# Performance work log

Hardware: AMD Instinct MI355X
Metric: run time of the kernel (lower is better)

## Reference

```python
import jax, jax.numpy as jnp
import numpy as np

# dims: batch, q-heads, kv-heads, seq, head_dim, block size, window (kv blocks per q block)
B, H, KVH, S, D = 2, 16, 4, 4096, 64
BLK, W = 64, 8
G = H // KVH          # heads per group = 4
NQ = S // BLK         # 64 query blocks
L = W * BLK           # flattened kv window per q block = 512


def setup_inputs() -> dict:
    key = jax.random.key(0)
    k0, k1, k2, k3 = jax.random.split(key, 4)
    q = jax.random.normal(k0, (B, H, S, D), jnp.float32)
    k = jax.random.normal(k1, (B, KVH, S, D), jnp.float32)
    v = jax.random.normal(k2, (B, KVH, S, D), jnp.float32)
    # standard alibi slopes 2^(-8i/H)
    alibi_slopes = jnp.asarray(2.0 ** (-8.0 * np.arange(1, H + 1) / H), jnp.float32)
    # contiguous segments via sorted random ids
    segment_ids = jnp.sort(jax.random.randint(k3, (B, S), 0, 8, jnp.int32), axis=-1)
    # causal sliding window: q block qb attends to kv blocks [qb-W+1, qb]; -1 = invalid
    qb = np.arange(NQ)[:, None]
    bi = qb - (W - 1) + np.arange(W)[None, :]
    block_indices = jnp.asarray(np.where(bi < 0, -1, bi), jnp.int32)  # [NQ, W]
    return {"q": q, "k": k, "v": v, "alibi_slopes": alibi_slopes,
            "segment_ids": segment_ids, "block_indices": block_indices}


def reference(q, k, v, alibi_slopes, segment_ids, block_indices):
    scale = jnp.float32(1.0 / np.sqrt(D))
    NEG = jnp.float32(-1e30)

    qg = q.reshape(B, KVH, G, NQ, BLK, D)          # GQA grouping
    kb = k.reshape(B, KVH, NQ, BLK, D)
    vb = v.reshape(B, KVH, NQ, BLK, D)

    safe = jnp.clip(block_indices, 0)               # [NQ, W]
    kg = kb[:, :, safe]                             # [B,KVH,NQ,W,BLK,D] gathered kv blocks
    vg = vb[:, :, safe]

    pos_m = (jnp.arange(NQ) * BLK)[:, None] + jnp.arange(BLK)             # [NQ,BM]
    pos_n = safe[:, :, None] * BLK + jnp.arange(BLK)[None, None, :]       # [NQ,W,BN]

    valid = (block_indices >= 0)[:, None, :, None]                        # [NQ,1,W,1]
    causal = pos_m[:, :, None, None] >= pos_n[:, None, :, :]              # [NQ,BM,W,BN]
    seg_q = segment_ids.reshape(B, NQ, BLK)
    seg_k = jnp.take(segment_ids, pos_n.reshape(-1), axis=1).reshape(B, NQ, W, BLK)
    same_seg = (seg_q[:, :, :, None, None] == seg_k[:, :, None, :, :]) & (seg_q[:, :, :, None, None] >= 0)
    mask = ((valid & causal)[None] & same_seg)                            # [B,NQ,BM,W,BN]
    maskb = mask.reshape(B, 1, 1, NQ, BLK, L)                             # broadcast over KVH,G

    scores = jnp.einsum('bkgqmd,bkqwnd->bkgqmwn', qg, kg) * scale         # [B,KVH,G,NQ,BM,W,BN]
    pos_diff = jnp.abs(pos_m[:, :, None, None] - pos_n[:, None, :, :]).astype(jnp.float32)
    scores = scores - alibi_slopes.reshape(KVH, G)[None, :, :, None, None, None, None] * pos_diff
    scores = scores.reshape(B, KVH, G, NQ, BLK, L)
    scores = jnp.where(maskb, scores, NEG)

    row_max = jnp.max(scores, axis=-1, keepdims=True)
    p = jnp.where(maskb, jnp.exp(scores - row_max), 0.0)
    l = jnp.sum(p, axis=-1, keepdims=True)                                # [B,KVH,G,NQ,BM,1]
    vf = vg.reshape(B, KVH, NQ, L, D)
    acc = jnp.einsum('bkgqml,bkqld->bkgqmd', p, vf)
    out = jnp.where(l > 0, acc / jnp.where(l > 0, l, 1.0), 0.0)           # zero rows with no valid kv
    return out.reshape(B, H, S, D)
```

## Files before the change

kernel.cpp:

```cpp
#include <hip/hip_runtime.h>
#include <hip/hip_bf16.h>

#define NKVH 4
#define SEQ 4096
#define BLK 64
#define NW 8
#define NQB 64

typedef __attribute__((ext_vector_type(8))) short bf16x8;
typedef __attribute__((ext_vector_type(4))) float f32x4;

__device__ __forceinline__ unsigned pkbf(unsigned lo, unsigned hi) {
  return __builtin_amdgcn_perm(hi + 0x8000u, lo + 0x8000u, 0x07060302u);
}

__device__ __forceinline__ void gload16(const void* g, void* l) {
  __builtin_amdgcn_global_load_lds(
      (const __attribute__((address_space(1))) void*)g,
      (__attribute__((address_space(3))) void*)l, 16, 0, 0);
}

__global__ __launch_bounds__(256, 2)
void prep_kernel(const float* __restrict__ kp, const float* __restrict__ vp,
                 short* __restrict__ kw, short* __restrict__ vt)
{
  const int ki = blockIdx.x, kvh = blockIdx.y, b = blockIdx.z;
  const size_t base = (((size_t)(b*NKVH + kvh)*SEQ) + (size_t)ki*BLK)*64;
  __shared__ float sk[64][72];
  __shared__ float sv[64][72];
  const int t = threadIdx.x;
  #pragma unroll
  for (int it = 0; it < 4; ++it) {
    const int i = t + it*256;
    const int row = i >> 4, c4 = i & 15;
    float4 a = *(const float4*)(kp + base + row*64 + c4*4);
    *(float4*)&sk[row][c4*4] = a;
    float4 v = *(const float4*)(vp + base + row*64 + c4*4);
    *(float4*)&sv[row][c4*4] = v;
  }
  __syncthreads();
  #pragma unroll
  for (int it = 0; it < 2; ++it) {
    const int o = t + it*256;
    const int s = o >> 8, fd = (o >> 6) & 3, lg = (o >> 4) & 3, lr = o & 15;
    const int krow = 8*(lr >> 2) + (lr & 3) + 4*(fd & 1) + 32*(fd >> 1);
    const float* src = &sk[krow][s*32 + lg*8];
    uint4 w;
    w.x = pkbf(__float_as_uint(src[0]), __float_as_uint(src[1]));
    w.y = pkbf(__float_as_uint(src[2]), __float_as_uint(src[3]));
    w.z = pkbf(__float_as_uint(src[4]), __float_as_uint(src[5]));
    w.w = pkbf(__float_as_uint(src[6]), __float_as_uint(src[7]));
    *(uint4*)(kw + base + (size_t)o*8) = w;
    const int d = fd*16 + lr;
    const int n0 = s*32 + lg*8;
    uint4 u;
    u.x = pkbf(__float_as_uint(sv[n0+0][d]), __float_as_uint(sv[n0+1][d]));
    u.y = pkbf(__float_as_uint(sv[n0+2][d]), __float_as_uint(sv[n0+3][d]));
    u.z = pkbf(__float_as_uint(sv[n0+4][d]), __float_as_uint(sv[n0+5][d]));
    u.w = pkbf(__float_as_uint(sv[n0+6][d]), __float_as_uint(sv[n0+7][d]));
    *(uint4*)(vt + base + (size_t)o*8) = u;
  }
}

__global__ __launch_bounds__(256, 2)
void sattn_kernel(const float* __restrict__ qp, const short* __restrict__ kw,
                  const short* __restrict__ vt, const float* __restrict__ alibi,
                  const int* __restrict__ seg, const int* __restrict__ bidx,
                  float* __restrict__ outp)
{
  const int raw = blockIdx.x;
  const int xcd = raw & 7, li = raw >> 3;
  const int b = xcd >> 2, kvh = xcd & 3;
  const int qb = li & 63, hp = li >> 6;

  const int tid = threadIdx.x;
  const int wave = tid >> 6, lane = tid & 63;
  const int lr = lane & 15, lg = lane >> 4;
  const int wh = wave & 1, wq = wave >> 1;
  const int head = kvh*4 + hp*2 + wh;

  __shared__ short klds[2][4096];
  __shared__ short vlds[2][4096];

  int kis[NW];
  #pragma unroll
  for (int i = 0; i < NW; ++i) kis[i] = bidx[qb*NW + i];

  int m_glob[2], mloc[2], sq[2];
  #pragma unroll
  for (int g = 0; g < 2; ++g) {
    mloc[g] = (wq*2 + g)*16 + lr;
    m_glob[g] = qb*BLK + mloc[g];
    sq[g] = seg[b*SEQ + m_glob[g]];
  }
  const float LOG2E = 1.4426950408889634f;
  const float nslope = -alibi[head] * LOG2E;

  const short* kbase = kw + ((size_t)(b*NKVH + kvh)*SEQ)*64;
  const short* vbase = vt + ((size_t)(b*NKVH + kvh)*SEQ)*64;

  auto STAGE = [&](int buf, int wi) {
    const int ki = kis[wi] < 0 ? 0 : kis[wi];
    const char* ksrc = (const char*)(kbase + (size_t)ki*4096);
    const char* vsrc = (const char*)(vbase + (size_t)ki*4096);
    gload16(ksrc + tid*16,        (char*)&klds[buf][0] + wave*1024);
    gload16(ksrc + 4096 + tid*16, (char*)&klds[buf][0] + 4096 + wave*1024);
    gload16(vsrc + tid*16,        (char*)&vlds[buf][0] + wave*1024);
    gload16(vsrc + 4096 + tid*16, (char*)&vlds[buf][0] + 4096 + wave*1024);
  };

  STAGE(0, 0);

  bf16x8 qf[2][2];
  {
    const float qs = 0.125f * LOG2E;
    #pragma unroll
    for (int g = 0; g < 2; ++g) {
      const float* qrow = qp + (((size_t)b*16 + head)*SEQ + m_glob[g])*64;
      #pragma unroll
      for (int s = 0; s < 2; ++s) {
        float4 a = *(const float4*)(qrow + s*32 + lg*8);
        float4 c = *(const float4*)(qrow + s*32 + lg*8 + 4);
        union { unsigned u[4]; bf16x8 v; } cv;
        cv.u[0] = pkbf(__float_as_uint(a.x*qs), __float_as_uint(a.y*qs));
        cv.u[1] = pkbf(__float_as_uint(a.z*qs), __float_as_uint(a.w*qs));
        cv.u[2] = pkbf(__float_as_uint(c.x*qs), __float_as_uint(c.y*qs));
        cv.u[3] = pkbf(__float_as_uint(c.z*qs), __float_as_uint(c.w*qs));
        qf[g][s] = cv.v;
      }
    }
  }

  union { unsigned short us[8]; bf16x8 v; } one_u;
  #pragma unroll
  for (int i = 0; i < 8; ++i) one_u.us[i] = 0x3F80;
  const bf16x8 onesf = one_u.v;

  f32x4 oacc[2][4], osum[2];
  #pragma unroll
  for (int g = 0; g < 2; ++g) {
    f32x4 z = {0.f,0.f,0.f,0.f};
    osum[g] = z;
    #pragma unroll
    for (int dt = 0; dt < 4; ++dt) oacc[g][dt] = z;
  }

  __syncthreads();

  int cur = 0;
  #pragma unroll
  for (int wi = 0; wi < NW; ++wi) {
    if (wi + 1 < NW) STAGE(cur ^ 1, wi + 1);
    const int ki = kis[wi];
    if (ki >= 0) {
      int skr[4][4];
      #pragma unroll
      for (int f = 0; f < 4; ++f) {
        const int nb = lg*8 + 4*(f & 1) + 32*(f >> 1);
        const int4 s4 = *(const int4*)(seg + b*SEQ + ki*BLK + nb);
        skr[f][0] = s4.x; skr[f][1] = s4.y; skr[f][2] = s4.z; skr[f][3] = s4.w;
      }

      f32x4 sacc[2][4];
      #pragma unroll
      for (int g = 0; g < 2; ++g)
        #pragma unroll
        for (int f = 0; f < 4; ++f) { f32x4 z = {0.f,0.f,0.f,0.f}; sacc[g][f] = z; }
      #pragma unroll
      for (int s = 0; s < 2; ++s) {
        bf16x8 kf[4];
        #pragma unroll
        for (int f = 0; f < 4; ++f)
          kf[f] = *(const bf16x8*)&klds[cur][(s*256 + f*64 + lane)*8];
        __builtin_amdgcn_s_setprio(1);
        #pragma unroll
        for (int f = 0; f < 4; ++f)
          sacc[0][f] = __builtin_amdgcn_mfma_f32_16x16x32_bf16(kf[f], qf[0][s], sacc[0][f], 0, 0, 0);
        #pragma unroll
        for (int f = 0; f < 4; ++f)
          sacc[1][f] = __builtin_amdgcn_mfma_f32_16x16x32_bf16(kf[f], qf[1][s], sacc[1][f], 0, 0, 0);
        __builtin_amdgcn_s_setprio(0);
      }

      unsigned pk[2][4][2];
      #pragma unroll
      for (int g = 0; g < 2; ++g) {
        const float fdmb = (float)(m_glob[g] - ki*BLK);
        #pragma unroll
        for (int f = 0; f < 4; ++f) {
          const int nb = lg*8 + 4*(f & 1) + 32*(f >> 1);
          const float fbase = fdmb - (float)nb;
          float p[4];
          #pragma unroll
          for (int r = 0; r < 4; ++r) {
            bool dead = (skr[f][r] != sq[g]);
            if (wi == NW-1) dead = dead || ((nb + r) > mloc[g]);
            const float pd = dead ? 3.0e34f : (fbase - (float)r);
            p[r] = __builtin_amdgcn_exp2f(fmaf(nslope, pd, sacc[g][f][r]));
          }
          pk[g][f][0] = pkbf(__float_as_uint(p[0]), __float_as_uint(p[1]));
          pk[g][f][1] = pkbf(__float_as_uint(p[2]), __float_as_uint(p[3]));
        }
      }

      #pragma unroll
      for (int s = 0; s < 2; ++s) {
        bf16x8 vf[4];
        #pragma unroll
        for (int dt = 0; dt < 4; ++dt)
          vf[dt] = *(const bf16x8*)&vlds[cur][(s*256 + dt*64 + lane)*8];
        union { unsigned u[4]; bf16x8 v; } pf0, pf1;
        pf0.u[0] = pk[0][2*s][0]; pf0.u[1] = pk[0][2*s][1];
        pf0.u[2] = pk[0][2*s+1][0]; pf0.u[3] = pk[0][2*s+1][1];
        pf1.u[0] = pk[1][2*s][0]; pf1.u[1] = pk[1][2*s][1];
        pf1.u[2] = pk[1][2*s+1][0]; pf1.u[3] = pk[1][2*s+1][1];
        __builtin_amdgcn_s_setprio(1);
        #pragma unroll
        for (int dt = 0; dt < 4; ++dt)
          oacc[0][dt] = __builtin_amdgcn_mfma_f32_16x16x32_bf16(vf[dt], pf0.v, oacc[0][dt], 0, 0, 0);
        #pragma unroll
        for (int dt = 0; dt < 4; ++dt)
          oacc[1][dt] = __builtin_amdgcn_mfma_f32_16x16x32_bf16(vf[dt], pf1.v, oacc[1][dt], 0, 0, 0);
        osum[0] = __builtin_amdgcn_mfma_f32_16x16x32_bf16(onesf, pf0.v, osum[0], 0, 0, 0);
        osum[1] = __builtin_amdgcn_mfma_f32_16x16x32_bf16(onesf, pf1.v, osum[1], 0, 0, 0);
        __builtin_amdgcn_s_setprio(0);
      }
    }
    __syncthreads();
    cur ^= 1;
  }

  #pragma unroll
  for (int g = 0; g < 2; ++g) {
    const float lrow = osum[g][0];
    const float inv = lrow > 0.f ? 1.f/lrow : 0.f;
    float* dst = outp + (((size_t)b*16 + head)*SEQ + m_glob[g])*64;
    #pragma unroll
    for (int dt = 0; dt < 4; ++dt) {
      float4 o;
      o.x = oacc[g][dt][0]*inv; o.y = oacc[g][dt][1]*inv;
      o.z = oacc[g][dt][2]*inv; o.w = oacc[g][dt][3]*inv;
      *(float4*)&dst[dt*16 + lg*4] = o;
    }
  }
}

extern "C" void kernel_launch(void* const* d_in, const int* in_sizes, int n_in,
                              void* d_out, int out_size, void* d_ws, size_t ws_size,
                              hipStream_t stream) {
  const float* q    = (const float*)d_in[0];
  const float* k    = (const float*)d_in[1];
  const float* v    = (const float*)d_in[2];
  const float* al   = (const float*)d_in[3];
  const int*   sg   = (const int*)d_in[4];
  const int*   bi   = (const int*)d_in[5];
  short* kws  = (short*)d_ws;
  short* vtws = (short*)((char*)d_ws + (size_t)(1u<<22));
  dim3 pgrid(NQB, NKVH, 2);
  prep_kernel<<<pgrid, 256, 0, stream>>>(k, v, kws, vtws);
  sattn_kernel<<<dim3(1024), 256, 0, stream>>>(q, kws, vtws, al, sg, bi, (float*)d_out);
}
```

Before: 46.58 us.

## Software-pipeline QK and PV across kv blocks with triple-buffered V

Restructures the window loop so the QK^T MFMAs and softmax of block wi run alongside the PV MFMAs of block wi-1. Each block's packed probabilities are held in a two-slot register buffer, V gets a third LDS buffer, and the final block's PV is done in an epilogue. Invalid blocks are no longer skipped with a branch; they are clamped to block 0 and fully masked, which removes divergence but spends compute on dead blocks. The aim is to overlap exp/VALU work with MFMA work, at the cost of more registers and LDS.

```diff
diff --git a/kernel.cpp b/kernel.cpp
--- a/kernel.cpp
+++ b/kernel.cpp
@@ -80,7 +80,7 @@
   const int head = kvh*4 + hp*2 + wh;
 
   __shared__ short klds[2][4096];
-  __shared__ short vlds[2][4096];
+  __shared__ short vlds[3][4096];
 
   int kis[NW];
   #pragma unroll
@@ -99,17 +99,17 @@
   const short* kbase = kw + ((size_t)(b*NKVH + kvh)*SEQ)*64;
   const short* vbase = vt + ((size_t)(b*NKVH + kvh)*SEQ)*64;
 
-  auto STAGE = [&](int buf, int wi) {
+  auto STAGE = [&](int kbuf, int vbuf, int wi) {
     const int ki = kis[wi] < 0 ? 0 : kis[wi];
     const char* ksrc = (const char*)(kbase + (size_t)ki*4096);
     const char* vsrc = (const char*)(vbase + (size_t)ki*4096);
-    gload16(ksrc + tid*16,        (char*)&klds[buf][0] + wave*1024);
-    gload16(ksrc + 4096 + tid*16, (char*)&klds[buf][0] + 4096 + wave*1024);
-    gload16(vsrc + tid*16,        (char*)&vlds[buf][0] + wave*1024);
-    gload16(vsrc + 4096 + tid*16, (char*)&vlds[buf][0] + 4096 + wave*1024);
+    gload16(ksrc + tid*16,        (char*)&klds[kbuf][0] + wave*1024);
+    gload16(ksrc + 4096 + tid*16, (char*)&klds[kbuf][0] + 4096 + wave*1024);
+    gload16(vsrc + tid*16,        (char*)&vlds[vbuf][0] + wave*1024);
+    gload16(vsrc + 4096 + tid*16, (char*)&vlds[vbuf][0] + 4096 + wave*1024);
   };
 
-  STAGE(0, 0);
+  STAGE(0, 0, 0);
 
   bf16x8 qf[2][2];
   {
@@ -145,47 +145,76 @@
     for (int dt = 0; dt < 4; ++dt) oacc[g][dt] = z;
   }
 
+  unsigned pkbuf[2][2][4][2];
+
   __syncthreads();
 
-  int cur = 0;
   #pragma unroll
   for (int wi = 0; wi < NW; ++wi) {
-    if (wi + 1 < NW) STAGE(cur ^ 1, wi + 1);
-    const int ki = kis[wi];
-    if (ki >= 0) {
-      int skr[4][4];
-      #pragma unroll
-      for (int f = 0; f < 4; ++f) {
-        const int nb = lg*8 + 4*(f & 1) + 32*(f >> 1);
-        const int4 s4 = *(const int4*)(seg + b*SEQ + ki*BLK + nb);
-        skr[f][0] = s4.x; skr[f][1] = s4.y; skr[f][2] = s4.z; skr[f][3] = s4.w;
-      }
-
-      f32x4 sacc[2][4];
-      #pragma unroll
-      for (int g = 0; g < 2; ++g)
-        #pragma unroll
-        for (int f = 0; f < 4; ++f) { f32x4 z = {0.f,0.f,0.f,0.f}; sacc[g][f] = z; }
+    if (wi + 1 < NW) STAGE((wi+1)&1, (wi+1)%3, wi+1);
+
+    const int kvi = kis[wi];
+    const int kcl = kvi < 0 ? 0 : kvi;
+
+    int skr[4][4];
+    #pragma unroll
+    for (int f = 0; f < 4; ++f) {
+      const int nb = lg*8 + 4*(f & 1) + 32*(f >> 1);
+      const int4 s4 = *(const int4*)(seg + b*SEQ + kcl*BLK + nb);
+      skr[f][0] = s4.x; skr[f][1] = s4.y; skr[f][2] = s4.z; skr[f][3] = s4.w;
+    }
+
+    f32x4 sacc[2][4];
+    #pragma unroll
+    for (int g = 0; g < 2; ++g)
+      #pragma unroll
+      for (int f = 0; f < 4; ++f) { f32x4 z = {0.f,0.f,0.f,0.f}; sacc[g][f] = z; }
+    #pragma unroll
+    for (int s = 0; s < 2; ++s) {
+      bf16x8 kf[4];
+      #pragma unroll
+      for (int f = 0; f < 4; ++f)
+        kf[f] = *(const bf16x8*)&klds[wi&1][(s*256 + f*64 + lane)*8];
+      __builtin_amdgcn_s_setprio(1);
+      #pragma unroll
+      for (int f = 0; f < 4; ++f)
+        sacc[0][f] = __builtin_amdgcn_mfma_f32_16x16x32_bf16(kf[f], qf[0][s], sacc[0][f], 0, 0, 0);
+      #pragma unroll
+      for (int f = 0; f < 4; ++f)
+        sacc[1][f] = __builtin_amdgcn_mfma_f32_16x16x32_bf16(kf[f], qf[1][s], sacc[1][f], 0, 0, 0);
+      __builtin_amdgcn_s_setprio(0);
+    }
+
+    if (wi > 0) {
       #pragma unroll
       for (int s = 0; s < 2; ++s) {
-        bf16x8 kf[4];
-        #pragma unroll
-        for (int f = 0; f < 4; ++f)
-          kf[f] = *(const bf16x8*)&klds[cur][(s*256 + f*64 + lane)*8];
+        bf16x8 vf[4];
+        #pragma unroll
+        for (int dt = 0; dt < 4; ++dt)
+          vf[dt] = *(const bf16x8*)&vlds[(wi-1)%3][(s*256 + dt*64 + lane)*8];
+        union { unsigned u[4]; bf16x8 v; } pf0, pf1;
+        pf0.u[0] = pkbuf[(wi-1)&1][0][2*s][0]; pf0.u[1] = pkbuf[(wi-1)&1][0][2*s][1];
+        pf0.u[2] = pkbuf[(wi-1)&1][0][2*s+1][0]; pf0.u[3] = pkbuf[(wi-1)&1][0][2*s+1][1];
+        pf1.u[0] = pkbuf[(wi-1)&1][1][2*s][0]; pf1.u[1] = pkbuf[(wi-1)&1][1][2*s][1];
+        pf1.u[2] = pkbuf[(wi-1)&1][1][2*s+1][0]; pf1.u[3] = pkbuf[(wi-1)&1][1][2*s+1][1];
         __builtin_amdgcn_s_setprio(1);
         #pragma unroll
-        for (int f = 0; f < 4; ++f)
-          sacc[0][f] = __builtin_amdgcn_mfma_f32_16x16x32_bf16(kf[f], qf[0][s], sacc[0][f], 0, 0, 0);
-        #pragma unroll
-        for (int f = 0; f < 4; ++f)
-          sacc[1][f] = __builtin_amdgcn_mfma_f32_16x16x32_bf16(kf[f], qf[1][s], sacc[1][f], 0, 0, 0);
+        for (int dt = 0; dt < 4; ++dt)
+          oacc[0][dt] = __builtin_amdgcn_mfma_f32_16x16x32_bf16(vf[dt], pf0.v, oacc[0][dt], 0, 0, 0);
+        #pragma unroll
+        for (int dt = 0; dt < 4; ++dt)
+          oacc[1][dt] = __builtin_amdgcn_mfma_f32_16x16x32_bf16(vf[dt], pf1.v, oacc[1][dt], 0, 0, 0);
+        osum[0] = __builtin_amdgcn_mfma_f32_16x16x32_bf16(onesf, pf0.v, osum[0], 0, 0, 0);
+        osum[1] = __builtin_amdgcn_mfma_f32_16x16x32_bf16(onesf, pf1.v, osum[1], 0, 0, 0);
         __builtin_amdgcn_s_setprio(0);
       }
-
-      unsigned pk[2][4][2];
+    }
+
+    {
+      const bool wdead = (kvi < 0);
       #pragma unroll
       for (int g = 0; g < 2; ++g) {
-        const float fdmb = (float)(m_glob[g] - ki*BLK);
+        const float fdmb = (float)(m_glob[g] - kcl*BLK);
         #pragma unroll
         for (int f = 0; f < 4; ++f) {
           const int nb = lg*8 + 4*(f & 1) + 32*(f >> 1);
@@ -193,41 +222,38 @@
           float p[4];
           #pragma unroll
           for (int r = 0; r < 4; ++r) {
-            bool dead = (skr[f][r] != sq[g]);
+            bool dead = wdead || (skr[f][r] != sq[g]);
             if (wi == NW-1) dead = dead || ((nb + r) > mloc[g]);
             const float pd = dead ? 3.0e34f : (fbase - (float)r);
             p[r] = __builtin_amdgcn_exp2f(fmaf(nslope, pd, sacc[g][f][r]));
           }
-          pk[g][f][0] = pkbf(__float_as_uint(p[0]), __float_as_uint(p[1]));
-          pk[g][f][1] = pkbf(__float_as_uint(p[2]), __float_as_uint(p[3]));
+          pkbuf[wi&1][g][f][0] = pkbf(__float_as_uint(p[0]), __float_as_uint(p[1]));
+          pkbuf[wi&1][g][f][1] = pkbf(__float_as_uint(p[2]), __float_as_uint(p[3]));
         }
       }
-
-      #pragma unroll
-      for (int s = 0; s < 2; ++s) {
-        bf16x8 vf[4];
-        #pragma unroll
-        for (int dt = 0; dt < 4; ++dt)
-          vf[dt] = *(const bf16x8*)&vlds[cur][(s*256 + dt*64 + lane)*8];
-        union { unsigned u[4]; bf16x8 v; } pf0, pf1;
-        pf0.u[0] = pk[0][2*s][0]; pf0.u[1] = pk[0][2*s][1];
-        pf0.u[2] = pk[0][2*s+1][0]; pf0.u[3] = pk[0][2*s+1][1];
-        pf1.u[0] = pk[1][2*s][0]; pf1.u[1] = pk[1][2*s][1];
-        pf1.u[2] = pk[1][2*s+1][0]; pf1.u[3] = pk[1][2*s+1][1];
-        __builtin_amdgcn_s_setprio(1);
-        #pragma unroll
-        for (int dt = 0; dt < 4; ++dt)
-          oacc[0][dt] = __builtin_amdgcn_mfma_f32_16x16x32_bf16(vf[dt], pf0.v, oacc[0][dt], 0, 0, 0);
-        #pragma unroll
-        for (int dt = 0; dt < 4; ++dt)
-          oacc[1][dt] = __builtin_amdgcn_mfma_f32_16x16x32_bf16(vf[dt], pf1.v, oacc[1][dt], 0, 0, 0);
-        osum[0] = __builtin_amdgcn_mfma_f32_16x16x32_bf16(onesf, pf0.v, osum[0], 0, 0, 0);
-        osum[1] = __builtin_amdgcn_mfma_f32_16x16x32_bf16(onesf, pf1.v, osum[1], 0, 0, 0);
-        __builtin_amdgcn_s_setprio(0);
-      }
     }
     __syncthreads();
-    cur ^= 1;
+  }
+
+  #pragma unroll
+  for (int s = 0; s < 2; ++s) {
+    bf16x8 vf[4];
+    #pragma unroll
+    for (int dt = 0; dt < 4; ++dt)
+      vf[dt] = *(const bf16x8*)&vlds[1][(s*256 + dt*64 + lane)*8];
+    union { unsigned u[4]; bf16x8 v; } pf0, pf1;
+    pf0.u[0] = pkbuf[1][0][2*s][0]; pf0.u[1] = pkbuf[1][0][2*s][1];
+    pf0.u[2] = pkbuf[1][0][2*s+1][0]; pf0.u[3] = pkbuf[1][0][2*s+1][1];
+    pf1.u[0] = pkbuf[1][1][2*s][0]; pf1.u[1] = pkbuf[1][1][2*s][1];
+    pf1.u[2] = pkbuf[1][1][2*s+1][0]; pf1.u[3] = pkbuf[1][1][2*s+1][1];
+    #pragma unroll
+    for (int dt = 0; dt < 4; ++dt)
+      oacc[0][dt] = __builtin_amdgcn_mfma_f32_16x16x32_bf16(vf[dt], pf0.v, oacc[0][dt], 0, 0, 0);
+    #pragma unroll
+    for (int dt = 0; dt < 4; ++dt)
+      oacc[1][dt] = __builtin_amdgcn_mfma_f32_16x16x32_bf16(vf[dt], pf1.v, oacc[1][dt], 0, 0, 0);
+    osum[0] = __builtin_amdgcn_mfma_f32_16x16x32_bf16(onesf, pf0.v, osum[0], 0, 0, 0);
+    osum[1] = __builtin_amdgcn_mfma_f32_16x16x32_bf16(onesf, pf1.v, osum[1], 0, 0, 0);
   }
 
   #pragma unroll
```

After: 48.10 us. +3.3%, slower.

## Replace per-key segment loads with segment-start range mask and explicit barriers

Applied to the files above, without the earlier changes.

Adds a small kernel that records the first position of each segment id, relying on segments being contiguous. The attention kernel then builds its mask from one unsigned range compare per key, and no longer loads segment ids for every kv block. It also zeroes masked probabilities after the exp, precomputes the per-lane alibi offsets, and swaps __syncthreads for an explicit vmcnt wait plus barrier, skipping the barrier after the last iteration. This removes global segment loads and compare work from the inner loop, at the cost of an extra tiny kernel launch and an assumption that segments are contiguous runs.

```diff
diff --git a/kernel.cpp b/kernel.cpp
--- a/kernel.cpp
+++ b/kernel.cpp
@@ -18,6 +18,21 @@
   __builtin_amdgcn_global_load_lds(
       (const __attribute__((address_space(1))) void*)g,
       (__attribute__((address_space(3))) void*)l, 16, 0, 0);
+}
+
+__global__ __launch_bounds__(256, 2)
+void segscan_kernel(const int* __restrict__ seg, int* __restrict__ fo)
+{
+  const int b = blockIdx.x;
+  __shared__ int fol[8];
+  if (threadIdx.x < 8) fol[threadIdx.x] = 0x7FFFFFFF;
+  __syncthreads();
+  for (int i = threadIdx.x; i < SEQ; i += 256) {
+    const int v = seg[b*SEQ + i];
+    if (i == 0 || seg[b*SEQ + i - 1] != v) atomicMin(&fol[v], i);
+  }
+  __syncthreads();
+  if (threadIdx.x < 8) fo[b*8 + threadIdx.x] = fol[threadIdx.x];
 }
 
 __global__ __launch_bounds__(256, 2)
@@ -66,7 +81,7 @@
 void sattn_kernel(const float* __restrict__ qp, const short* __restrict__ kw,
                   const short* __restrict__ vt, const float* __restrict__ alibi,
                   const int* __restrict__ seg, const int* __restrict__ bidx,
-                  float* __restrict__ outp)
+                  const int* __restrict__ fo, float* __restrict__ outp)
 {
   const int raw = blockIdx.x;
   const int xcd = raw & 7, li = raw >> 3;
@@ -86,15 +101,20 @@
   #pragma unroll
   for (int i = 0; i < NW; ++i) kis[i] = bidx[qb*NW + i];
 
-  int m_glob[2], mloc[2], sq[2];
+  int m_glob[2], lo[2];
+  unsigned relm[2];
   #pragma unroll
   for (int g = 0; g < 2; ++g) {
-    mloc[g] = (wq*2 + g)*16 + lr;
-    m_glob[g] = qb*BLK + mloc[g];
-    sq[g] = seg[b*SEQ + m_glob[g]];
+    m_glob[g] = qb*BLK + (wq*2 + g)*16 + lr;
+    const int sv = seg[b*SEQ + m_glob[g]];
+    lo[g] = fo[b*8 + sv];
+    relm[g] = (unsigned)(m_glob[g] - lo[g]);
   }
   const float LOG2E = 1.4426950408889634f;
   const float nslope = -alibi[head] * LOG2E;
+  float nsr[4];
+  #pragma unroll
+  for (int r = 0; r < 4; ++r) nsr[r] = -nslope * (float)r;
 
   const short* kbase = kw + ((size_t)(b*NKVH + kvh)*SEQ)*64;
   const short* vbase = vt + ((size_t)(b*NKVH + kvh)*SEQ)*64;
@@ -145,22 +165,15 @@
     for (int dt = 0; dt < 4; ++dt) oacc[g][dt] = z;
   }
 
-  __syncthreads();
-
-  int cur = 0;
+  asm volatile("s_waitcnt vmcnt(0)" ::: "memory");
+  __builtin_amdgcn_s_barrier();
+
   #pragma unroll
   for (int wi = 0; wi < NW; ++wi) {
+    const int cur = wi & 1;
     if (wi + 1 < NW) STAGE(cur ^ 1, wi + 1);
-    const int ki = kis[wi];
-    if (ki >= 0) {
-      int skr[4][4];
-      #pragma unroll
-      for (int f = 0; f < 4; ++f) {
-        const int nb = lg*8 + 4*(f & 1) + 32*(f >> 1);
-        const int4 s4 = *(const int4*)(seg + b*SEQ + ki*BLK + nb);
-        skr[f][0] = s4.x; skr[f][1] = s4.y; skr[f][2] = s4.z; skr[f][3] = s4.w;
-      }
-
+    const int kvi = kis[wi];
+    if (kvi >= 0) {
       f32x4 sacc[2][4];
       #pragma unroll
       for (int g = 0; g < 2; ++g)
@@ -185,18 +198,18 @@
       unsigned pk[2][4][2];
       #pragma unroll
       for (int g = 0; g < 2; ++g) {
-        const float fdmb = (float)(m_glob[g] - ki*BLK);
         #pragma unroll
         for (int f = 0; f < 4; ++f) {
           const int nb = lg*8 + 4*(f & 1) + 32*(f >> 1);
-          const float fbase = fdmb - (float)nb;
+          const int n0 = kvi*BLK + nb;
+          const unsigned nrel0 = (unsigned)(n0 - lo[g]);
+          const float af = nslope * (float)(m_glob[g] - n0);
           float p[4];
           #pragma unroll
           for (int r = 0; r < 4; ++r) {
-            bool dead = (skr[f][r] != sq[g]);
-            if (wi == NW-1) dead = dead || ((nb + r) > mloc[g]);
-            const float pd = dead ? 3.0e34f : (fbase - (float)r);
-            p[r] = __builtin_amdgcn_exp2f(fmaf(nslope, pd, sacc[g][f][r]));
+            const bool live = (nrel0 + (unsigned)r) <= relm[g];
+            const float pv = __builtin_amdgcn_exp2f(sacc[g][f][r] + af + nsr[r]);
+            p[r] = live ? pv : 0.f;
           }
           pk[g][f][0] = pkbf(__float_as_uint(p[0]), __float_as_uint(p[1]));
           pk[g][f][1] = pkbf(__float_as_uint(p[2]), __float_as_uint(p[3]));
@@ -226,8 +239,10 @@
         __builtin_amdgcn_s_setprio(0);
       }
     }
-    __syncthreads();
-    cur ^= 1;
+    if (wi + 1 < NW) {
+      asm volatile("s_waitcnt vmcnt(0)" ::: "memory");
+      __builtin_amdgcn_s_barrier();
+    }
   }
 
   #pragma unroll
@@ -256,7 +271,9 @@
   const int*   bi   = (const int*)d_in[5];
   short* kws  = (short*)d_ws;
   short* vtws = (short*)((char*)d_ws + (size_t)(1u<<22));
+  int*   fo   = (int*)((char*)d_ws + (size_t)(1u<<23));
+  segscan_kernel<<<dim3(2), 256, 0, stream>>>(sg, fo);
   dim3 pgrid(NQB, NKVH, 2);
   prep_kernel<<<pgrid, 256, 0, stream>>>(k, v, kws, vtws);
-  sattn_kernel<<<dim3(1024), 256, 0, stream>>>(q, kws, vtws, al, sg, bi, (float*)d_out);
-}
+  sattn_kernel<<<dim3(1024), 256, 0, stream>>>(q, kws, vtws, al, sg, bi, fo, (float*)d_out);
+}
```

After: 52.12 us. 11.9% more time.
